# Optimization experiments

Measured on AMD Instinct MI355X. Metric: run time of the kernel, lower is better.

The kernel has to match this reference:

```python
import jax, jax.numpy as jnp
import numpy as np

N = 50000
E = 800000
IN_C, HID, LAT = 256, 128, 64


def setup_inputs() -> dict:
    key = jax.random.key(0)
    ks = jax.random.split(key, 8)
    x = jax.random.normal(ks[0], (N, IN_C), dtype=jnp.float32)
    edge_index = jax.random.randint(ks[1], (2, E), 0, N, dtype=jnp.int64)
    # Glorot-ish scaled weights (PyG GCNConv: Linear weight + separate bias)
    W1 = jax.random.normal(ks[2], (IN_C, HID), dtype=jnp.float32) / np.sqrt(IN_C)
    b1 = jnp.zeros((HID,), dtype=jnp.float32)
    Wmu = jax.random.normal(ks[3], (HID, LAT), dtype=jnp.float32) / np.sqrt(HID)
    bmu = jnp.zeros((LAT,), dtype=jnp.float32)
    Wlv = jax.random.normal(ks[4], (HID, LAT), dtype=jnp.float32) / np.sqrt(HID)
    blv = jnp.zeros((LAT,), dtype=jnp.float32)
    return {"x": x, "edge_index": edge_index, "W1": W1, "b1": b1,
            "Wmu": Wmu, "bmu": bmu, "Wlv": Wlv, "blv": blv}


def gcn_conv(x, edge_index, W, b):
    """PyG GCNConv: add self-loops, sym-normalize, transform, scatter-add."""
    n = x.shape[0]
    loop = jnp.arange(n, dtype=edge_index.dtype)
    row = jnp.concatenate([edge_index[0], loop])  # source
    col = jnp.concatenate([edge_index[1], loop])  # target
    deg = jax.ops.segment_sum(jnp.ones_like(col, dtype=x.dtype), col, num_segments=n)
    dinv = jax.lax.rsqrt(jnp.maximum(deg, 1e-12))  # deg >= 1 due to self-loops
    norm = dinv[row] * dinv[col]                   # [E+N]
    h = x @ W                                      # transform first (smaller width)
    msg = h[row] * norm[:, None]                   # [E+N, out] gathered messages
    out = jax.ops.segment_sum(msg, col, num_segments=n)
    return out + b


def reference(x, edge_index, W1, b1, Wmu, bmu, Wlv, blv):
    h = jax.nn.relu(gcn_conv(x, edge_index, W1, b1))
    # dropout p=0.0 -> identity
    mu = gcn_conv(h, edge_index, Wmu, bmu)
    logvar = gcn_conv(h, edge_index, Wlv, blv)
    return (mu, logvar)
```

## Files before the change

kernel.cpp:

```cpp
#include <hip/hip_runtime.h>
#include <stdint.h>

#define NN   50000
#define NE   800000
#define INC  256
#define HID  128
#define LAT  64

typedef unsigned short u16;
typedef short v8s __attribute__((ext_vector_type(8)));
typedef float v4f __attribute__((ext_vector_type(4)));

#define SLAB_OFF 0
#define OFFS_OFF 802816
#define W1P_OFF  881216
#define W2P_OFF  897600
#define G1_OFF   905792

#define NBIN        196
#define OFFS_STRIDE 200
#define NSLAB       784

#define G2_OFFU  8388608
#define C2_CNT   8388608
#define C2_DINV  8438608
#define C2_BKT   8488608

#define GB    782

__device__ __forceinline__ u16 f2b(float f) {
    union { float f; uint32_t i; } c; c.f = f;
    uint32_t r = c.i + 0x7FFF + ((c.i >> 16) & 1);
    return (u16)(r >> 16);
}
__device__ __forceinline__ float blo(unsigned u) { return __uint_as_float(u << 16); }
__device__ __forceinline__ float bhi(unsigned u) { return __uint_as_float(u & 0xffff0000u); }

__device__ void pack1_body(const float* __restrict__ W1, u16* __restrict__ W1P, int b) {
    int tg = b * 256 + threadIdx.x;
    int ks = tg >> 9, rem = tg & 511;
    int nt = rem >> 6, lane = rem & 63;
    int quad = lane >> 4, l15 = lane & 15;
    u16 o[8];
    #pragma unroll
    for (int j = 0; j < 8; j++)
        o[j] = f2b(W1[(long)(ks * 32 + quad * 8 + j) * HID + nt * 16 + l15]);
    *(ushort4*)(W1P + (long)tg * 8)     = make_ushort4(o[0], o[1], o[2], o[3]);
    *(ushort4*)(W1P + (long)tg * 8 + 4) = make_ushort4(o[4], o[5], o[6], o[7]);
}

__device__ void pack2_body(const float* __restrict__ Wmu, const float* __restrict__ Wlv,
                           u16* __restrict__ W2P, int b) {
    int tg = b * 256 + threadIdx.x;
    int ks = tg >> 9, rem = tg & 511;
    int nt = rem >> 6, lane = rem & 63;
    int quad = lane >> 4, l15 = lane & 15;
    const float* W = (nt < 4) ? Wmu : Wlv;
    int ntl = (nt < 4) ? nt : nt - 4;
    u16 o[8];
    #pragma unroll
    for (int j = 0; j < 8; j++)
        o[j] = f2b(W[(long)(ks * 32 + quad * 8 + j) * LAT + ntl * 16 + l15]);
    *(ushort4*)(W2P + (long)tg * 8)     = make_ushort4(o[0], o[1], o[2], o[3]);
    *(ushort4*)(W2P + (long)tg * 8 + 4) = make_ushort4(o[4], o[5], o[6], o[7]);
}

__global__ __launch_bounds__(256) void k_fusedA(unsigned* csr, const float* W1,
        const float* Wmu, const float* Wlv) {
    int b = blockIdx.x;
    if (b < 16) pack1_body(W1, (u16*)(csr + W1P_OFF), b);
    else pack2_body(Wmu, Wlv, (u16*)(csr + W2P_OFF), b - 16);
}

__device__ void gemm1_body(const float* __restrict__ xbuf,
        const unsigned* __restrict__ csr, u16* __restrict__ g1, int blk) {
    const u16* W1P = (const u16*)(csr + W1P_OFF);
    int tid = threadIdx.x;
    int lane = tid & 63, w = tid >> 6;
    int quad = lane >> 4, l15 = lane & 15;
    int m0 = blk * 64 + w * 16;
    int arow = m0 + l15;
    int arc = arow < NN ? arow : NN - 1;
    const float* ap = xbuf + (long)arc * INC + quad * 8;
    const v8s* bp = (const v8s*)W1P;
    v4f acc[8];
    #pragma unroll
    for (int t = 0; t < 8; t++) acc[t] = (v4f){0.f, 0.f, 0.f, 0.f};

    #pragma unroll 1
    for (int ks = 0; ks < 8; ks++) {
        float4 a0 = *(const float4*)(ap + ks * 32);
        float4 a1 = *(const float4*)(ap + ks * 32 + 4);
        v8s af;
        af[0] = (short)f2b(a0.x); af[1] = (short)f2b(a0.y);
        af[2] = (short)f2b(a0.z); af[3] = (short)f2b(a0.w);
        af[4] = (short)f2b(a1.x); af[5] = (short)f2b(a1.y);
        af[6] = (short)f2b(a1.z); af[7] = (short)f2b(a1.w);
        #pragma unroll
        for (int t = 0; t < 8; t++) {
            v8s bf = bp[(ks * 8 + t) * 64 + lane];
            acc[t] = __builtin_amdgcn_mfma_f32_16x16x32_bf16(af, bf, acc[t], 0, 0, 0);
        }
    }
    #pragma unroll
    for (int r = 0; r < 4; r++) {
        int rr = m0 + quad * 4 + r;
        if (rr < NN) {
            u16* dst = g1 + (long)rr * HID + l15;
            #pragma unroll
            for (int t = 0; t < 8; t++) dst[t * 16] = f2b(acc[t][r]);
        }
    }
}

__device__ void part_body(const int* __restrict__ row, const int* __restrict__ col,
                          unsigned* __restrict__ csr, int id) {
    __shared__ int hist[256];
    __shared__ int scanbuf[256];
    __shared__ unsigned recs[1024];
    int tid = threadIdx.x;
    int base = id * 1024;
    hist[tid] = 0;
    __syncthreads();
    int v[4], u[4];
    #pragma unroll
    for (int i = 0; i < 4; i++) {
        int e = base + i * 256 + tid;
        if (e < NE) {
            v[i] = col[e]; u[i] = row[e];
            atomicAdd(&hist[v[i] >> 8], 1);
        } else v[i] = -1;
    }
    __syncthreads();
    int x = hist[tid];
    scanbuf[tid] = x;
    __syncthreads();
    for (int s = 1; s < 256; s <<= 1) {
        int y = (tid >= s) ? scanbuf[tid - s] : 0;
        __syncthreads();
        scanbuf[tid] += y;
        __syncthreads();
    }
    int excl = scanbuf[tid] - x;
    u16* offs = (u16*)(csr + OFFS_OFF) + (long)id * OFFS_STRIDE;
    if (tid <= NBIN) offs[tid] = (u16)excl;
    hist[tid] = excl;
    __syncthreads();
    #pragma unroll
    for (int i = 0; i < 4; i++) {
        if (v[i] >= 0) {
            int slot = atomicAdd(&hist[v[i] >> 8], 1);
            recs[slot] = (unsigned)u[i] | ((unsigned)(v[i] & 255) << 16);
        }
    }
    __syncthreads();
    unsigned* slab = csr + SLAB_OFF + (long)id * 1024;
    #pragma unroll
    for (int i = 0; i < 4; i++) slab[i * 256 + tid] = recs[i * 256 + tid];
}

__global__ __launch_bounds__(256) void k_fusedB(const float* __restrict__ xbuf,
        unsigned* __restrict__ csr, u16* __restrict__ g1,
        const int* __restrict__ row, const int* __restrict__ col) {
    int b = blockIdx.x;
    int g = b >> 3, r = b & 7;
    int id = (g >> 1) * 8 + r;
    if (g & 1) part_body(row, col, csr, id);
    else gemm1_body(xbuf, csr, g1, id);
}

__global__ __launch_bounds__(256) void k_merge(const unsigned* __restrict__ csr,
        unsigned* __restrict__ xb) {
    __shared__ int cnt_lds[256];
    __shared__ u16 bkt_lds[256 * 64];
    int tid = threadIdx.x;
    int bin = blockIdx.x;
    cnt_lds[tid] = 0;
    __syncthreads();
    const u16* offs = (const u16*)(csr + OFFS_OFF);
    const unsigned* slab = csr + SLAB_OFF;
    for (int s = tid; s < NSLAB; s += 256) {
        int st = offs[s * OFFS_STRIDE + bin];
        int en = offs[s * OFFS_STRIDE + bin + 1];
        for (int j = st; j < en; j++) {
            unsigned r = slab[s * 1024 + j];
            int vlo = (int)(r >> 16);
            int slot = atomicAdd(&cnt_lds[vlo], 1);
            if (slot < 64) bkt_lds[(vlo << 6) + slot] = (u16)(r & 0xffffu);
        }
    }
    __syncthreads();
    int* cnt2 = (int*)(xb + C2_CNT);
    float* dinv = (float*)(xb + C2_DINV);
    u16* bkt2 = (u16*)(xb + C2_BKT);
    int v0 = bin << 8;
    {
        int v = v0 + tid;
        if (v < NN) {
            int deg = cnt_lds[tid];
            int cn = deg < 64 ? deg : 64;
            cnt2[v] = cn;
            dinv[v] = rsqrtf((float)(deg + 1));
        }
    }
    const uint4* src = (const uint4*)bkt_lds;
    #pragma unroll
    for (int i = 0; i < 8; i++) {
        int idx = i * 256 + tid;
        int node = idx >> 3;
        if (v0 + node < NN)
            ((uint4*)(bkt2 + ((long)(v0 + node) << 6)))[idx & 7] = src[idx];
    }
}

#define ACC8(P, D, W) if (P) { \
    a0 += D * blo(W.x); a1 += D * bhi(W.x); a2 += D * blo(W.y); a3 += D * bhi(W.y); \
    a4 += D * blo(W.z); a5 += D * bhi(W.z); a6 += D * blo(W.w); a7 += D * bhi(W.w); }
#define RED(S) \
    a0 += __shfl_xor(a0, S); a1 += __shfl_xor(a1, S); a2 += __shfl_xor(a2, S); \
    a3 += __shfl_xor(a3, S); a4 += __shfl_xor(a4, S); a5 += __shfl_xor(a5, S); \
    a6 += __shfl_xor(a6, S); a7 += __shfl_xor(a7, S);

__global__ __launch_bounds__(256) void k_gather1(const u16* __restrict__ g1,
        const unsigned* __restrict__ xb, const float* __restrict__ b1,
        u16* __restrict__ h) {
    int tid = threadIdx.x;
    int lane = tid & 63, w = tid >> 6;
    int v = blockIdx.x * 4 + w;
    int q = lane >> 4, c = lane & 15;
    const int* cnt2 = (const int*)(xb + C2_CNT);
    const float* dinv = (const float*)(xb + C2_DINV);
    const u16* bkt2 = (const u16*)(xb + C2_BKT);
    int cn = cnt2[v];
    float dvv = dinv[v];
    int idx = (lane < cn) ? (int)bkt2[(v << 6) + lane] : 0;
    float dvu = dinv[idx];
    float a0 = 0.f, a1 = 0.f, a2 = 0.f, a3 = 0.f, a4 = 0.f, a5 = 0.f, a6 = 0.f, a7 = 0.f;
    if (q == 0) {
        uint4 wv = *(const uint4*)(g1 + (long)v * HID + c * 8);
        a0 = dvv * blo(wv.x); a1 = dvv * bhi(wv.x); a2 = dvv * blo(wv.y); a3 = dvv * bhi(wv.y);
        a4 = dvv * blo(wv.z); a5 = dvv * bhi(wv.z); a6 = dvv * blo(wv.w); a7 = dvv * bhi(wv.w);
    }
    for (int t = 0; t < cn; t += 16) {
        int t0 = t + q, t1 = t0 + 4, t2 = t0 + 8, t3 = t0 + 12;
        bool p0 = t0 < cn, p1 = t1 < cn, p2 = t2 < cn, p3 = t3 < cn;
        int u0 = __shfl(idx, t0), u1 = __shfl(idx, t1),
            u2 = __shfl(idx, t2), u3 = __shfl(idx, t3);
        float d0 = __shfl(dvu, t0), d1 = __shfl(dvu, t1),
              d2 = __shfl(dvu, t2), d3 = __shfl(dvu, t3);
        uint4 w0, w1, w2, w3;
        if (p0) w0 = *(const uint4*)(g1 + (long)u0 * HID + c * 8);
        if (p1) w1 = *(const uint4*)(g1 + (long)u1 * HID + c * 8);
        if (p2) w2 = *(const uint4*)(g1 + (long)u2 * HID + c * 8);
        if (p3) w3 = *(const uint4*)(g1 + (long)u3 * HID + c * 8);
        ACC8(p0, d0, w0)
        ACC8(p1, d1, w1)
        ACC8(p2, d2, w2)
        ACC8(p3, d3, w3)
    }
    RED(16)
    RED(32)
    if (q == 0) {
        int j = c * 8;
        float r[8] = {a0, a1, a2, a3, a4, a5, a6, a7};
        unsigned p[4];
        #pragma unroll
        for (int i = 0; i < 4; i++) {
            float x0 = dvv * r[2 * i]     + b1[j + 2 * i];
            float x1 = dvv * r[2 * i + 1] + b1[j + 2 * i + 1];
            x0 = x0 > 0.f ? x0 : 0.f;
            x1 = x1 > 0.f ? x1 : 0.f;
            p[i] = (unsigned)f2b(x0) | ((unsigned)f2b(x1) << 16);
        }
        uint4 o; o.x = p[0]; o.y = p[1]; o.z = p[2]; o.w = p[3];
        *(uint4*)(h + (long)v * HID + j) = o;
    }
}

__global__ __launch_bounds__(256) void k_gemm2(const u16* __restrict__ h,
        const unsigned* __restrict__ csr, u16* __restrict__ g2) {
    const u16* W2P = (const u16*)(csr + W2P_OFF);
    int tid = threadIdx.x;
    int lane = tid & 63, w = tid >> 6;
    int quad = lane >> 4, l15 = lane & 15;
    int m0 = blockIdx.x * 64 + w * 16;
    int arow = m0 + l15;
    int arc = arow < NN ? arow : NN - 1;
    const u16* ap = h + (long)arc * HID + quad * 8;
    const v8s* bp = (const v8s*)W2P;
    v4f acc[8];
    #pragma unroll
    for (int t = 0; t < 8; t++) acc[t] = (v4f){0.f, 0.f, 0.f, 0.f};

    #pragma unroll 1
    for (int ks = 0; ks < 4; ks++) {
        v8s af = *(const v8s*)(ap + ks * 32);
        #pragma unroll
        for (int t = 0; t < 8; t++) {
            v8s bf = bp[(ks * 8 + t) * 64 + lane];
            acc[t] = __builtin_amdgcn_mfma_f32_16x16x32_bf16(af, bf, acc[t], 0, 0, 0);
        }
    }
    #pragma unroll
    for (int r = 0; r < 4; r++) {
        int rr = m0 + quad * 4 + r;
        if (rr < NN) {
            u16* dst = g2 + (long)rr * HID + l15;
            #pragma unroll
            for (int t = 0; t < 8; t++) dst[t * 16] = f2b(acc[t][r]);
        }
    }
}

__global__ __launch_bounds__(256) void k_gather2(const u16* __restrict__ g2,
        const unsigned* __restrict__ xb, const float* __restrict__ bmu,
        const float* __restrict__ blv, float* __restrict__ out) {
    int tid = threadIdx.x;
    int lane = tid & 63, w = tid >> 6;
    int v = blockIdx.x * 4 + w;
    int q = lane >> 4, c = lane & 15;
    const int* cnt2 = (const int*)(xb + C2_CNT);
    const float* dinv = (const float*)(xb + C2_DINV);
    const u16* bkt2 = (const u16*)(xb + C2_BKT);
    int cn = cnt2[v];
    float dvv = dinv[v];
    int idx = (lane < cn) ? (int)bkt2[(v << 6) + lane] : 0;
    float dvu = dinv[idx];
    float a0 = 0.f, a1 = 0.f, a2 = 0.f, a3 = 0.f, a4 = 0.f, a5 = 0.f, a6 = 0.f, a7 = 0.f;
    if (q == 0) {
        uint4 wv = *(const uint4*)(g2 + (long)v * HID + c * 8);
        a0 = dvv * blo(wv.x); a1 = dvv * bhi(wv.x); a2 = dvv * blo(wv.y); a3 = dvv * bhi(wv.y);
        a4 = dvv * blo(wv.z); a5 = dvv * bhi(wv.z); a6 = dvv * blo(wv.w); a7 = dvv * bhi(wv.w);
    }
    for (int t = 0; t < cn; t += 16) {
        int t0 = t + q, t1 = t0 + 4, t2 = t0 + 8, t3 = t0 + 12;
        bool p0 = t0 < cn, p1 = t1 < cn, p2 = t2 < cn, p3 = t3 < cn;
        int u0 = __shfl(idx, t0), u1 = __shfl(idx, t1),
            u2 = __shfl(idx, t2), u3 = __shfl(idx, t3);
        float d0 = __shfl(dvu, t0), d1 = __shfl(dvu, t1),
              d2 = __shfl(dvu, t2), d3 = __shfl(dvu, t3);
        uint4 w0, w1, w2, w3;
        if (p0) w0 = *(const uint4*)(g2 + (long)u0 * HID + c * 8);
        if (p1) w1 = *(const uint4*)(g2 + (long)u1 * HID + c * 8);
        if (p2) w2 = *(const uint4*)(g2 + (long)u2 * HID + c * 8);
        if (p3) w3 = *(const uint4*)(g2 + (long)u3 * HID + c * 8);
        ACC8(p0, d0, w0)
        ACC8(p1, d1, w1)
        ACC8(p2, d2, w2)
        ACC8(p3, d3, w3)
    }
    RED(16)
    RED(32)
    if (q == 0) {
        float r[8] = {a0, a1, a2, a3, a4, a5, a6, a7};
        if (c < 8) {
            int j = c * 8;
            float4 o0 = make_float4(dvv * r[0] + bmu[j],     dvv * r[1] + bmu[j + 1],
                                    dvv * r[2] + bmu[j + 2], dvv * r[3] + bmu[j + 3]);
            float4 o1 = make_float4(dvv * r[4] + bmu[j + 4], dvv * r[5] + bmu[j + 5],
                                    dvv * r[6] + bmu[j + 6], dvv * r[7] + bmu[j + 7]);
            float* dst = out + (long)v * LAT + j;
            *(float4*)dst = o0;
            *(float4*)(dst + 4) = o1;
        } else {
            int j = c * 8 - 64;
            float4 o0 = make_float4(dvv * r[0] + blv[j],     dvv * r[1] + blv[j + 1],
                                    dvv * r[2] + blv[j + 2], dvv * r[3] + blv[j + 3]);
            float4 o1 = make_float4(dvv * r[4] + blv[j + 4], dvv * r[5] + blv[j + 5],
                                    dvv * r[6] + blv[j + 6], dvv * r[7] + blv[j + 7]);
            float* dst = out + (long)NN * LAT + (long)v * LAT + j;
            *(float4*)dst = o0;
            *(float4*)(dst + 4) = o1;
        }
    }
}

extern "C" void kernel_launch(void* const* d_in, const int* in_sizes, int n_in,
                              void* d_out, int out_size, void* d_ws, size_t ws_size,
                              hipStream_t stream) {
    float* xbuf = (float*)d_in[0];
    const int* ei  = (const int*)d_in[1];
    const float* W1  = (const float*)d_in[2];
    const float* b1  = (const float*)d_in[3];
    const float* Wmu = (const float*)d_in[4];
    const float* bmu = (const float*)d_in[5];
    const float* Wlv = (const float*)d_in[6];
    const float* blv = (const float*)d_in[7];
    const int* row = ei;
    const int* col = ei + NE;

    unsigned* csr = (unsigned*)d_out;
    u16* g1   = (u16*)(csr + G1_OFF);
    u16* hbuf = (u16*)xbuf;
    u16* g2   = (u16*)xbuf + G2_OFFU;
    unsigned* xb = (unsigned*)xbuf;

    k_fusedA<<<24, 256, 0, stream>>>(csr, W1, Wmu, Wlv);

    k_fusedB<<<1568, 256, 0, stream>>>(xbuf, csr, g1, row, col);
    k_merge <<<NBIN, 256, 0, stream>>>(csr, xb);
    k_gather1<<<NN / 4, 256, 0, stream>>>(g1, xb, b1, hbuf);

    k_gemm2 <<<GB, 256, 0, stream>>>(hbuf, csr, g2);
    k_gather2<<<NN / 4, 256, 0, stream>>>(g2, xb, bmu, blv, (float*)d_out);
}
```

Measured before the change: 223.7 us.

## Hoist GEMM operand loads, widen gather unroll, co-locate gemm1 and partition per block

Both GEMM bodies now issue all A-operand loads up front into registers before the MFMA loop, so memory latency overlaps instead of being serialized per k-step. The gather loops in both aggregation kernels process 8 neighbor rows per lane group per iteration instead of 4, putting more independent loads in flight. The fused kernel now runs gemm1 and the edge partition in the same block (784 blocks) instead of interleaving separate blocks, which changes scheduling and raises per-block work and register pressure.

```diff
diff --git a/kernel.cpp b/kernel.cpp
--- a/kernel.cpp
+++ b/kernel.cpp
@@ -87,10 +87,15 @@
     #pragma unroll
     for (int t = 0; t < 8; t++) acc[t] = (v4f){0.f, 0.f, 0.f, 0.f};
 
-    #pragma unroll 1
+    float4 A[16];
+    #pragma unroll
     for (int ks = 0; ks < 8; ks++) {
-        float4 a0 = *(const float4*)(ap + ks * 32);
-        float4 a1 = *(const float4*)(ap + ks * 32 + 4);
+        A[2 * ks]     = *(const float4*)(ap + ks * 32);
+        A[2 * ks + 1] = *(const float4*)(ap + ks * 32 + 4);
+    }
+    #pragma unroll
+    for (int ks = 0; ks < 8; ks++) {
+        float4 a0 = A[2 * ks], a1 = A[2 * ks + 1];
         v8s af;
         af[0] = (short)f2b(a0.x); af[1] = (short)f2b(a0.y);
         af[2] = (short)f2b(a0.z); af[3] = (short)f2b(a0.w);
@@ -163,10 +168,8 @@
         unsigned* __restrict__ csr, u16* __restrict__ g1,
         const int* __restrict__ row, const int* __restrict__ col) {
     int b = blockIdx.x;
-    int g = b >> 3, r = b & 7;
-    int id = (g >> 1) * 8 + r;
-    if (g & 1) part_body(row, col, csr, id);
-    else gemm1_body(xbuf, csr, g1, id);
+    if (b < GB) gemm1_body(xbuf, csr, g1, b);
+    part_body(row, col, csr, b);
 }
 
 __global__ __launch_bounds__(256) void k_merge(const unsigned* __restrict__ csr,
@@ -220,6 +223,37 @@
     a0 += __shfl_xor(a0, S); a1 += __shfl_xor(a1, S); a2 += __shfl_xor(a2, S); \
     a3 += __shfl_xor(a3, S); a4 += __shfl_xor(a4, S); a5 += __shfl_xor(a5, S); \
     a6 += __shfl_xor(a6, S); a7 += __shfl_xor(a7, S);
+
+#define GATHER_LOOP(SRC) \
+    for (int t = 0; t < cn; t += 32) { \
+        int t0 = t + q, t1 = t0 + 4, t2 = t0 + 8,  t3 = t0 + 12, \
+            t4 = t0 + 16, t5 = t0 + 20, t6 = t0 + 24, t7 = t0 + 28; \
+        bool p0 = t0 < cn, p1 = t1 < cn, p2 = t2 < cn, p3 = t3 < cn, \
+             p4 = t4 < cn, p5 = t5 < cn, p6 = t6 < cn, p7 = t7 < cn; \
+        int u0 = __shfl(idx, t0), u1 = __shfl(idx, t1), u2 = __shfl(idx, t2), \
+            u3 = __shfl(idx, t3), u4 = __shfl(idx, t4), u5 = __shfl(idx, t5), \
+            u6 = __shfl(idx, t6), u7 = __shfl(idx, t7); \
+        float d0 = __shfl(dvu, t0), d1 = __shfl(dvu, t1), d2 = __shfl(dvu, t2), \
+              d3 = __shfl(dvu, t3), d4 = __shfl(dvu, t4), d5 = __shfl(dvu, t5), \
+              d6 = __shfl(dvu, t6), d7 = __shfl(dvu, t7); \
+        uint4 w0, w1, w2, w3, w4, w5, w6, w7; \
+        if (p0) w0 = *(const uint4*)(SRC + (long)u0 * HID + c * 8); \
+        if (p1) w1 = *(const uint4*)(SRC + (long)u1 * HID + c * 8); \
+        if (p2) w2 = *(const uint4*)(SRC + (long)u2 * HID + c * 8); \
+        if (p3) w3 = *(const uint4*)(SRC + (long)u3 * HID + c * 8); \
+        if (p4) w4 = *(const uint4*)(SRC + (long)u4 * HID + c * 8); \
+        if (p5) w5 = *(const uint4*)(SRC + (long)u5 * HID + c * 8); \
+        if (p6) w6 = *(const uint4*)(SRC + (long)u6 * HID + c * 8); \
+        if (p7) w7 = *(const uint4*)(SRC + (long)u7 * HID + c * 8); \
+        ACC8(p0, d0, w0) \
+        ACC8(p1, d1, w1) \
+        ACC8(p2, d2, w2) \
+        ACC8(p3, d3, w3) \
+        ACC8(p4, d4, w4) \
+        ACC8(p5, d5, w5) \
+        ACC8(p6, d6, w6) \
+        ACC8(p7, d7, w7) \
+    }
 
 __global__ __launch_bounds__(256) void k_gather1(const u16* __restrict__ g1,
         const unsigned* __restrict__ xb, const float* __restrict__ b1,
@@ -241,23 +275,7 @@
         a0 = dvv * blo(wv.x); a1 = dvv * bhi(wv.x); a2 = dvv * blo(wv.y); a3 = dvv * bhi(wv.y);
         a4 = dvv * blo(wv.z); a5 = dvv * bhi(wv.z); a6 = dvv * blo(wv.w); a7 = dvv * bhi(wv.w);
     }
-    for (int t = 0; t < cn; t += 16) {
-        int t0 = t + q, t1 = t0 + 4, t2 = t0 + 8, t3 = t0 + 12;
-        bool p0 = t0 < cn, p1 = t1 < cn, p2 = t2 < cn, p3 = t3 < cn;
-        int u0 = __shfl(idx, t0), u1 = __shfl(idx, t1),
-            u2 = __shfl(idx, t2), u3 = __shfl(idx, t3);
-        float d0 = __shfl(dvu, t0), d1 = __shfl(dvu, t1),
-              d2 = __shfl(dvu, t2), d3 = __shfl(dvu, t3);
-        uint4 w0, w1, w2, w3;
-        if (p0) w0 = *(const uint4*)(g1 + (long)u0 * HID + c * 8);
-        if (p1) w1 = *(const uint4*)(g1 + (long)u1 * HID + c * 8);
-        if (p2) w2 = *(const uint4*)(g1 + (long)u2 * HID + c * 8);
-        if (p3) w3 = *(const uint4*)(g1 + (long)u3 * HID + c * 8);
-        ACC8(p0, d0, w0)
-        ACC8(p1, d1, w1)
-        ACC8(p2, d2, w2)
-        ACC8(p3, d3, w3)
-    }
+    GATHER_LOOP(g1)
     RED(16)
     RED(32)
     if (q == 0) {
@@ -292,13 +310,16 @@
     #pragma unroll
     for (int t = 0; t < 8; t++) acc[t] = (v4f){0.f, 0.f, 0.f, 0.f};
 
-    #pragma unroll 1
+    v8s af[4];
+    #pragma unroll
+    for (int ks = 0; ks < 4; ks++) af[ks] = *(const v8s*)(ap + ks * 32);
+
+    #pragma unroll
     for (int ks = 0; ks < 4; ks++) {
-        v8s af = *(const v8s*)(ap + ks * 32);
         #pragma unroll
         for (int t = 0; t < 8; t++) {
             v8s bf = bp[(ks * 8 + t) * 64 + lane];
-            acc[t] = __builtin_amdgcn_mfma_f32_16x16x32_bf16(af, bf, acc[t], 0, 0, 0);
+            acc[t] = __builtin_amdgcn_mfma_f32_16x16x32_bf16(af[ks], bf, acc[t], 0, 0, 0);
         }
     }
     #pragma unroll
@@ -332,23 +353,7 @@
         a0 = dvv * blo(wv.x); a1 = dvv * bhi(wv.x); a2 = dvv * blo(wv.y); a3 = dvv * bhi(wv.y);
         a4 = dvv * blo(wv.z); a5 = dvv * bhi(wv.z); a6 = dvv * blo(wv.w); a7 = dvv * bhi(wv.w);
     }
-    for (int t = 0; t < cn; t += 16) {
-        int t0 = t + q, t1 = t0 + 4, t2 = t0 + 8, t3 = t0 + 12;
-        bool p0 = t0 < cn, p1 = t1 < cn, p2 = t2 < cn, p3 = t3 < cn;
-        int u0 = __shfl(idx, t0), u1 = __shfl(idx, t1),
-            u2 = __shfl(idx, t2), u3 = __shfl(idx, t3);
-        float d0 = __shfl(dvu, t0), d1 = __shfl(dvu, t1),
-              d2 = __shfl(dvu, t2), d3 = __shfl(dvu, t3);
-        uint4 w0, w1, w2, w3;
-        if (p0) w0 = *(const uint4*)(g2 + (long)u0 * HID + c * 8);
-        if (p1) w1 = *(const uint4*)(g2 + (long)u1 * HID + c * 8);
-        if (p2) w2 = *(const uint4*)(g2 + (long)u2 * HID + c * 8);
-        if (p3) w3 = *(const uint4*)(g2 + (long)u3 * HID + c * 8);
-        ACC8(p0, d0, w0)
-        ACC8(p1, d1, w1)
-        ACC8(p2, d2, w2)
-        ACC8(p3, d3, w3)
-    }
+    GATHER_LOOP(g2)
     RED(16)
     RED(32)
     if (q == 0) {
@@ -397,7 +402,7 @@
 
     k_fusedA<<<24, 256, 0, stream>>>(csr, W1, Wmu, Wlv);
 
-    k_fusedB<<<1568, 256, 0, stream>>>(xbuf, csr, g1, row, col);
+    k_fusedB<<<NSLAB, 256, 0, stream>>>(xbuf, csr, g1, row, col);
     k_merge <<<NBIN, 256, 0, stream>>>(csr, xb);
     k_gather1<<<NN / 4, 256, 0, stream>>>(g1, xb, b1, hbuf);
 
```

Measured after the change: 223.1 us. No clear change (-0.3%).
